# Optimization experiments

Hardware: AMD Instinct MI355X
Metric: run time of the kernel (lower is better)

The kernel has to match this reference:

```python
import jax, jax.numpy as jnp
import numpy as np

B, T, H, N = 4, 512, 32, 64
D = H * N  # n_embd = 2048


def setup_inputs() -> dict:
    key = jax.random.key(0)
    ks = jax.random.split(key, 8)
    f = lambda kk: jax.random.normal(kk, (B, T, H, N), dtype=jnp.float32)
    r = f(ks[0])
    w = f(ks[1])
    k = f(ks[2])
    v = f(ks[3])
    iclr = f(ks[4])
    # int8-style quantized output projection: int values in [-128,127] + per-row scale
    w_out_q = jax.random.randint(ks[5], (D, D), -128, 128, dtype=jnp.int32)
    w_out_scale = jax.random.uniform(ks[6], (D,), dtype=jnp.float32) * 0.01
    return {"r": r, "w": w, "k": k, "v": v, "iclr": iclr,
            "w_out_q": w_out_q, "w_out_scale": w_out_scale}


def _wkv7(r, w, k, v, iclr):
    """RWKV x070 WKV scan. All inputs [B,T,H,N]; returns [B,T,H*N]."""
    decay = jnp.exp(-jnp.exp(w))  # per-channel decay in (0,1), x070 parameterization
    # kk = l2-normalized key direction; a = -kk (removal), b = kk * sigmoid(iclr) (write)
    kk = k * jax.lax.rsqrt(jnp.sum(k * k, axis=-1, keepdims=True) + 1e-12)
    a = -kk
    b = kk * jax.nn.sigmoid(iclr)

    def step(state, inp):
        # state: [B,H,N,N]; each inp element: [B,H,N]
        r_t, d_t, k_t, v_t, a_t, b_t = inp
        sa = jnp.einsum('bhij,bhj->bhi', state, a_t)
        state = (state * d_t[:, :, None, :]
                 + sa[..., None] * b_t[:, :, None, :]
                 + v_t[..., None] * k_t[:, :, None, :])
        y_t = jnp.einsum('bhij,bhj->bhi', state, r_t)
        return state, y_t

    tb = lambda x: jnp.swapaxes(x, 0, 1)  # [B,T,H,N] -> [T,B,H,N]
    state0 = jnp.zeros((B, H, N, N), dtype=r.dtype)
    _, y = jax.lax.scan(step, state0, (tb(r), tb(decay), tb(k), tb(v), tb(a), tb(b)))
    return jnp.swapaxes(y, 0, 1).reshape(B, T, H * N)


def reference(r, w, k, v, iclr, w_out_q, w_out_scale):
    y = _wkv7(r, w, k, v, iclr)               # [B,T,D]
    # inline dequant of quantized output projection (per-output-row scale)
    W = w_out_q.astype(jnp.float32) * w_out_scale[:, None]  # [D,D]
    return jnp.einsum('btd,od->bto', y, W)    # [B,T,D]
```

## Files before the change

### kernel.cpp

```cpp
#include <hip/hip_runtime.h>
#include <hip/hip_bf16.h>
#include <stdint.h>

#define B_ 4
#define T_ 512
#define H_ 32
#define N_ 64
#define D_ 2048
#define M_ (B_*T_)

typedef __attribute__((ext_vector_type(4))) float f32x4;
typedef __attribute__((ext_vector_type(8))) short short8;

template <int CTRL>
__device__ __forceinline__ float dpp_add(float x) {
    int t = __builtin_amdgcn_mov_dpp(__float_as_int(x), CTRL, 0xF, 0xF, true);
    return x + __int_as_float(t);
}
__device__ __forceinline__ float bfly16(float x) {
    x = dpp_add<0xB1>(x);
    x = dpp_add<0x4E>(x);
    x = dpp_add<0x141>(x);
    x = dpp_add<0x140>(x);
    return x;
}

__global__ __launch_bounds__(256) void conv_w(const int* __restrict__ q,
                                              __hip_bfloat16* __restrict__ o) {
    int i = (blockIdx.x * 256 + threadIdx.x) * 4;
    int4 qi = *(const int4*)(q + i);
    __hip_bfloat16 t[4];
    t[0] = __float2bfloat16((float)qi.x);
    t[1] = __float2bfloat16((float)qi.y);
    t[2] = __float2bfloat16((float)qi.z);
    t[3] = __float2bfloat16((float)qi.w);
    *(uint2*)(o + i) = *(uint2*)t;
}

__global__ __launch_bounds__(256) void precomp_t(
    const float* __restrict__ r, const float* __restrict__ w,
    const float* __restrict__ k, const float* __restrict__ v,
    const float* __restrict__ iclr,
    float* __restrict__ rT, float* __restrict__ kT, float* __restrict__ vT,
    float* __restrict__ decT, float* __restrict__ kkT, float* __restrict__ bbT) {
    int g = blockIdx.x * 4 + (threadIdx.x >> 6);
    int lane = threadIdx.x & 63;
    int b = g >> 14;
    int t = (g >> 5) & (T_ - 1);
    int h = g & 31;
    size_t si = (size_t)g * 64 + lane;
    size_t di = ((((size_t)b * H_ + h) * T_) + t) * 64 + lane;
    float rv = r[si], wv = w[si], kv = k[si], vv = v[si], av = iclr[si];
    float d = expf(-expf(wv));
    float ss = kv * kv;
#pragma unroll
    for (int m = 1; m < 64; m <<= 1) ss += __shfl_xor(ss, m, 64);
    float kkv = kv * rsqrtf(ss + 1e-12f);
    float bbv = kkv * (1.f / (1.f + expf(-av)));
    rT[di] = rv; kT[di] = kv; vT[di] = vv;
    decT[di] = d; kkT[di] = kkv; bbT[di] = bbv;
}

__device__ __forceinline__ void gld4(const float* g, float* l) {
    __builtin_amdgcn_global_load_lds(
        (const __attribute__((address_space(1))) unsigned int*)g,
        (__attribute__((address_space(3))) unsigned int*)l, 4, 0, 0);
}

__global__ __launch_bounds__(64, 2) void wkv_scan(
    const float* __restrict__ rT, const float* __restrict__ kT,
    const float* __restrict__ vT, const float* __restrict__ decT,
    const float* __restrict__ kkT, const float* __restrict__ bbT,
    __hip_bfloat16* __restrict__ y) {
    const int bh = blockIdx.x & 127;
    const int wv = blockIdx.x >> 7;
    const int b = bh >> 5, h = bh & 31;
    const int lane = threadIdx.x;
    const int jg = lane & 15;
    const int rl = lane >> 4;
    const int row = wv * 4 + rl;
    const int jb = jg * 4;

    __shared__ float ring[8][6][64];

    const size_t sbase = (size_t)bh * T_ * 64;
    const float* st[6] = { rT + sbase, kT + sbase, vT + sbase,
                           decT + sbase, kkT + sbase, bbT + sbase };

#pragma unroll
    for (int i = 0; i < 8; ++i)
#pragma unroll
        for (int s = 0; s < 6; ++s)
            gld4(st[s] + i * 64 + lane, &ring[i][s][0]);

    float S[4] = {0.f, 0.f, 0.f, 0.f};

    for (int t = 0; t < T_; ++t) {
        const int slot = t & 7;
        asm volatile("s_waitcnt vmcnt(42)" ::: "memory");

        f32x4 Rc = *(const f32x4*)(&ring[slot][0][jb]);
        f32x4 Kc = *(const f32x4*)(&ring[slot][1][jb]);
        float vcv =                  ring[slot][2][row];
        f32x4 Dc = *(const f32x4*)(&ring[slot][3][jb]);
        f32x4 Ac = *(const f32x4*)(&ring[slot][4][jb]);
        f32x4 Bc = *(const f32x4*)(&ring[slot][5][jb]);

        float s01 = fmaf(S[1], Ac[1], S[0] * Ac[0]);
        float s23 = fmaf(S[3], Ac[3], S[2] * Ac[2]);
        const float sa = -bfly16(s01 + s23);

        float t0 = fmaf(sa, Bc[0], vcv * Kc[0]);
        S[0] = fmaf(S[0], Dc[0], t0);
        float t1 = fmaf(sa, Bc[1], vcv * Kc[1]);
        S[1] = fmaf(S[1], Dc[1], t1);
        float y01 = fmaf(S[1], Rc[1], S[0] * Rc[0]);
        float t2 = fmaf(sa, Bc[2], vcv * Kc[2]);
        S[2] = fmaf(S[2], Dc[2], t2);
        float t3 = fmaf(sa, Bc[3], vcv * Kc[3]);
        S[3] = fmaf(S[3], Dc[3], t3);
        float y23 = fmaf(S[3], Rc[3], S[2] * Rc[2]);
        float ys = bfly16(y01 + y23);
        if (jg == 0)
            y[((size_t)b * T_ + t) * D_ + h * 64 + row] = __float2bfloat16(ys);

        asm volatile("" ::: "memory");
        int tp = t + 8; if (tp > T_ - 1) tp = T_ - 1;
#pragma unroll
        for (int s = 0; s < 6; ++s)
            gld4(st[s] + (size_t)tp * 64 + lane, &ring[slot][s][0]);
    }
}

__device__ __forceinline__ void gload_lds16(const __hip_bfloat16* g, ushort* l) {
    __builtin_amdgcn_global_load_lds(
        (const __attribute__((address_space(1))) unsigned int*)g,
        (__attribute__((address_space(3))) unsigned int*)l, 16, 0, 0);
}

__global__ __launch_bounds__(256, 1) void gemm_bt(
    const __hip_bfloat16* __restrict__ A,
    const __hip_bfloat16* __restrict__ Bq,
    const float* __restrict__ scale,
    float* __restrict__ C) {
    const int K = D_;
    __shared__ __align__(16) ushort As[128 * 64];
    __shared__ __align__(16) ushort Bs[128 * 64];

    const int tid = threadIdx.x;
    const int lane = tid & 63;
    const int wave = tid >> 6;
    const int wr = wave >> 1, wc = wave & 1;
    const int m0 = blockIdx.x * 128;
    const int n0 = blockIdx.y * 128;

    const int srow8 = lane >> 3;
    const int scol8 = (lane & 7) * 8;
    const int ml = lane & 15;
    const int kq = (lane >> 4) * 8;

    f32x4 acc[4][4] = {};

    for (int k0 = 0; k0 < K; k0 += 64) {
#pragma unroll
        for (int c = 0; c < 4; ++c) {
            int rbase = wave * 32 + c * 8;
            int row = rbase + srow8;
            gload_lds16(A  + (size_t)(m0 + row) * K + k0 + scol8, &As[rbase * 64]);
            gload_lds16(Bq + (size_t)(n0 + row) * K + k0 + scol8, &Bs[rbase * 64]);
        }
        __syncthreads();
#pragma unroll
        for (int ks = 0; ks < 2; ++ks) {
            short8 af[4], bf[4];
#pragma unroll
            for (int tm = 0; tm < 4; ++tm)
                af[tm] = *(const short8*)(&As[(wr * 64 + tm * 16 + ml) * 64 + ks * 32 + kq]);
#pragma unroll
            for (int tn = 0; tn < 4; ++tn)
                bf[tn] = *(const short8*)(&Bs[(wc * 64 + tn * 16 + ml) * 64 + ks * 32 + kq]);
#pragma unroll
            for (int tm = 0; tm < 4; ++tm)
#pragma unroll
                for (int tn = 0; tn < 4; ++tn)
                    acc[tm][tn] = __builtin_amdgcn_mfma_f32_16x16x32_bf16(
                        af[tm], bf[tn], acc[tm][tn], 0, 0, 0);
        }
        __syncthreads();
    }

#pragma unroll
    for (int tn = 0; tn < 4; ++tn) {
        int gn = n0 + wc * 64 + tn * 16 + ml;
        float sc = scale[gn];
#pragma unroll
        for (int tm = 0; tm < 4; ++tm) {
            int gm = m0 + wr * 64 + tm * 16 + (lane >> 4) * 4;
#pragma unroll
            for (int rg = 0; rg < 4; ++rg)
                C[(size_t)(gm + rg) * D_ + gn] = acc[tm][tn][rg] * sc;
        }
    }
}

extern "C" void kernel_launch(void* const* d_in, const int* in_sizes, int n_in,
                              void* d_out, int out_size, void* d_ws, size_t ws_size,
                              hipStream_t stream) {
    (void)in_sizes; (void)n_in; (void)out_size; (void)ws_size;
    const float* r  = (const float*)d_in[0];
    const float* w  = (const float*)d_in[1];
    const float* k  = (const float*)d_in[2];
    const float* v  = (const float*)d_in[3];
    const float* ic = (const float*)d_in[4];
    const int*   wq = (const int*)d_in[5];
    const float* sc = (const float*)d_in[6];
    float* out = (float*)d_out;

    const size_t NE = (size_t)B_ * T_ * H_ * N_;
    char* p = (char*)d_ws;
    __hip_bfloat16* yb = (__hip_bfloat16*)p;  p += (size_t)M_ * D_ * 2;
    __hip_bfloat16* wb = (__hip_bfloat16*)p;  p += (size_t)D_ * D_ * 2;
    float* rT   = (float*)p;  p += NE * 4;
    float* kT   = (float*)p;  p += NE * 4;
    float* vT   = (float*)p;  p += NE * 4;
    float* decT = (float*)p;  p += NE * 4;
    float* kkT  = (float*)p;  p += NE * 4;
    float* bbT  = (float*)p;

    conv_w   <<<dim3((D_ * D_) / (256 * 4)), dim3(256), 0, stream>>>(wq, wb);
    precomp_t<<<dim3(B_ * T_ * H_ / 4), dim3(256), 0, stream>>>(
        r, w, k, v, ic, rT, kT, vT, decT, kkT, bbT);
    wkv_scan <<<dim3(B_ * H_ * 16), dim3(64), 0, stream>>>(
        rT, kT, vT, decT, kkT, bbT, yb);
    gemm_bt  <<<dim3(M_ / 128, D_ / 128), dim3(256), 0, stream>>>(yb, wb, sc, out);
}
```

Measured before the change: 352.8 us.

## Pack scan inputs interleaved per timestep and prefetch 4-step chunks with 16B loads

The six precomputed per-channel streams now go into one interleaved buffer laid out as [bh][t][6][64]. This lets the scan kernel fetch four timesteps per group with 16-byte global-to-LDS loads into a double-buffered ring, instead of issuing six 4-byte loads every step. The weight conversion kernel is merged into the prep kernel through extra blocks, which saves one launch. The prefetch distance shrinks from 8 steps to between 4 and 8, which could expose load latency in the serial scan.

```diff
diff --git a/kernel.cpp b/kernel.cpp
--- a/kernel.cpp
+++ b/kernel.cpp
@@ -25,31 +25,35 @@
     return x;
 }
 
-__global__ __launch_bounds__(256) void conv_w(const int* __restrict__ q,
-                                              __hip_bfloat16* __restrict__ o) {
-    int i = (blockIdx.x * 256 + threadIdx.x) * 4;
-    int4 qi = *(const int4*)(q + i);
-    __hip_bfloat16 t[4];
-    t[0] = __float2bfloat16((float)qi.x);
-    t[1] = __float2bfloat16((float)qi.y);
-    t[2] = __float2bfloat16((float)qi.z);
-    t[3] = __float2bfloat16((float)qi.w);
-    *(uint2*)(o + i) = *(uint2*)t;
-}
-
-__global__ __launch_bounds__(256) void precomp_t(
+__device__ __forceinline__ void gld16(const float* g, float* l) {
+    __builtin_amdgcn_global_load_lds(
+        (const __attribute__((address_space(1))) unsigned int*)g,
+        (__attribute__((address_space(3))) unsigned int*)l, 16, 0, 0);
+}
+
+__global__ __launch_bounds__(256) void prep(
     const float* __restrict__ r, const float* __restrict__ w,
     const float* __restrict__ k, const float* __restrict__ v,
-    const float* __restrict__ iclr,
-    float* __restrict__ rT, float* __restrict__ kT, float* __restrict__ vT,
-    float* __restrict__ decT, float* __restrict__ kkT, float* __restrict__ bbT) {
+    const float* __restrict__ iclr, const int* __restrict__ q,
+    float* __restrict__ pk, __hip_bfloat16* __restrict__ o) {
+    if (blockIdx.x >= 16384) {
+        int i = ((blockIdx.x - 16384) * 256 + threadIdx.x) * 4;
+        int4 qi = *(const int4*)(q + i);
+        __hip_bfloat16 t[4];
+        t[0] = __float2bfloat16((float)qi.x);
+        t[1] = __float2bfloat16((float)qi.y);
+        t[2] = __float2bfloat16((float)qi.z);
+        t[3] = __float2bfloat16((float)qi.w);
+        *(uint2*)(o + i) = *(uint2*)t;
+        return;
+    }
     int g = blockIdx.x * 4 + (threadIdx.x >> 6);
     int lane = threadIdx.x & 63;
     int b = g >> 14;
     int t = (g >> 5) & (T_ - 1);
     int h = g & 31;
     size_t si = (size_t)g * 64 + lane;
-    size_t di = ((((size_t)b * H_ + h) * T_) + t) * 64 + lane;
+    size_t di = (((size_t)(b * H_ + h) * T_) + t) * 384 + lane;
     float rv = r[si], wv = w[si], kv = k[si], vv = v[si], av = iclr[si];
     float d = expf(-expf(wv));
     float ss = kv * kv;
@@ -57,21 +61,16 @@
     for (int m = 1; m < 64; m <<= 1) ss += __shfl_xor(ss, m, 64);
     float kkv = kv * rsqrtf(ss + 1e-12f);
     float bbv = kkv * (1.f / (1.f + expf(-av)));
-    rT[di] = rv; kT[di] = kv; vT[di] = vv;
-    decT[di] = d; kkT[di] = kkv; bbT[di] = bbv;
-}
-
-__device__ __forceinline__ void gld4(const float* g, float* l) {
-    __builtin_amdgcn_global_load_lds(
-        (const __attribute__((address_space(1))) unsigned int*)g,
-        (__attribute__((address_space(3))) unsigned int*)l, 4, 0, 0);
+    pk[di          ] = rv;
+    pk[di + 1 * 64 ] = kv;
+    pk[di + 2 * 64 ] = vv;
+    pk[di + 3 * 64 ] = d;
+    pk[di + 4 * 64 ] = kkv;
+    pk[di + 5 * 64 ] = bbv;
 }
 
 __global__ __launch_bounds__(64, 2) void wkv_scan(
-    const float* __restrict__ rT, const float* __restrict__ kT,
-    const float* __restrict__ vT, const float* __restrict__ decT,
-    const float* __restrict__ kkT, const float* __restrict__ bbT,
-    __hip_bfloat16* __restrict__ y) {
+    const float* __restrict__ pk, __hip_bfloat16* __restrict__ y) {
     const int bh = blockIdx.x & 127;
     const int wv = blockIdx.x >> 7;
     const int b = bh >> 5, h = bh & 31;
@@ -79,56 +78,66 @@
     const int jg = lane & 15;
     const int rl = lane >> 4;
     const int row = wv * 4 + rl;
-    const int jb = jg * 4;
-
-    __shared__ float ring[8][6][64];
-
-    const size_t sbase = (size_t)bh * T_ * 64;
-    const float* st[6] = { rT + sbase, kT + sbase, vT + sbase,
-                           decT + sbase, kkT + sbase, bbT + sbase };
-
-#pragma unroll
-    for (int i = 0; i < 8; ++i)
-#pragma unroll
-        for (int s = 0; s < 6; ++s)
-            gld4(st[s] + i * 64 + lane, &ring[i][s][0]);
+
+    __shared__ __align__(16) float ring[2 * 1536];
+
+    const float* src = pk + (size_t)bh * T_ * 384;
+
+#pragma unroll
+    for (int gg = 0; gg < 2; ++gg) {
+        const float* g0 = src + (size_t)gg * 1536 + lane * 4;
+        float* l0 = &ring[gg * 1536];
+#pragma unroll
+        for (int c = 0; c < 6; ++c)
+            gld16(g0 + c * 256, l0 + c * 256);
+    }
 
     float S[4] = {0.f, 0.f, 0.f, 0.f};
 
-    for (int t = 0; t < T_; ++t) {
-        const int slot = t & 7;
-        asm volatile("s_waitcnt vmcnt(42)" ::: "memory");
-
-        f32x4 Rc = *(const f32x4*)(&ring[slot][0][jb]);
-        f32x4 Kc = *(const f32x4*)(&ring[slot][1][jb]);
-        float vcv =                  ring[slot][2][row];
-        f32x4 Dc = *(const f32x4*)(&ring[slot][3][jb]);
-        f32x4 Ac = *(const f32x4*)(&ring[slot][4][jb]);
-        f32x4 Bc = *(const f32x4*)(&ring[slot][5][jb]);
-
-        float s01 = fmaf(S[1], Ac[1], S[0] * Ac[0]);
-        float s23 = fmaf(S[3], Ac[3], S[2] * Ac[2]);
-        const float sa = -bfly16(s01 + s23);
-
-        float t0 = fmaf(sa, Bc[0], vcv * Kc[0]);
-        S[0] = fmaf(S[0], Dc[0], t0);
-        float t1 = fmaf(sa, Bc[1], vcv * Kc[1]);
-        S[1] = fmaf(S[1], Dc[1], t1);
-        float y01 = fmaf(S[1], Rc[1], S[0] * Rc[0]);
-        float t2 = fmaf(sa, Bc[2], vcv * Kc[2]);
-        S[2] = fmaf(S[2], Dc[2], t2);
-        float t3 = fmaf(sa, Bc[3], vcv * Kc[3]);
-        S[3] = fmaf(S[3], Dc[3], t3);
-        float y23 = fmaf(S[3], Rc[3], S[2] * Rc[2]);
-        float ys = bfly16(y01 + y23);
-        if (jg == 0)
-            y[((size_t)b * T_ + t) * D_ + h * 64 + row] = __float2bfloat16(ys);
+    for (int g = 0; g < T_ / 4; ++g) {
+        const int slot = g & 1;
+        if (g == 0) { asm volatile("s_waitcnt vmcnt(6)"  ::: "memory"); }
+        else        { asm volatile("s_waitcnt vmcnt(10)" ::: "memory"); }
+        const float* rb0 = &ring[slot * 1536];
+
+#pragma unroll
+        for (int i = 0; i < 4; ++i) {
+            const int t = g * 4 + i;
+            const float* rb = rb0 + i * 384;
+
+            f32x4 Rc = *(const f32x4*)(rb + 0 * 64 + jg * 4);
+            f32x4 Kc = *(const f32x4*)(rb + 1 * 64 + jg * 4);
+            float vcv =                 rb[2 * 64 + row];
+            f32x4 Dc = *(const f32x4*)(rb + 3 * 64 + jg * 4);
+            f32x4 Ac = *(const f32x4*)(rb + 4 * 64 + jg * 4);
+            f32x4 Bc = *(const f32x4*)(rb + 5 * 64 + jg * 4);
+
+            float s01 = fmaf(S[1], Ac[1], S[0] * Ac[0]);
+            float s23 = fmaf(S[3], Ac[3], S[2] * Ac[2]);
+            const float sa = -bfly16(s01 + s23);
+
+            float t0 = fmaf(sa, Bc[0], vcv * Kc[0]);
+            S[0] = fmaf(S[0], Dc[0], t0);
+            float t1 = fmaf(sa, Bc[1], vcv * Kc[1]);
+            S[1] = fmaf(S[1], Dc[1], t1);
+            float y01 = fmaf(S[1], Rc[1], S[0] * Rc[0]);
+            float t2 = fmaf(sa, Bc[2], vcv * Kc[2]);
+            S[2] = fmaf(S[2], Dc[2], t2);
+            float t3 = fmaf(sa, Bc[3], vcv * Kc[3]);
+            S[3] = fmaf(S[3], Dc[3], t3);
+            float y23 = fmaf(S[3], Rc[3], S[2] * Rc[2]);
+            float ys = bfly16(y01 + y23);
+            if (jg == 0)
+                y[((size_t)b * T_ + t) * D_ + h * 64 + row] = __float2bfloat16(ys);
+        }
 
         asm volatile("" ::: "memory");
-        int tp = t + 8; if (tp > T_ - 1) tp = T_ - 1;
-#pragma unroll
-        for (int s = 0; s < 6; ++s)
-            gld4(st[s] + (size_t)tp * 64 + lane, &ring[slot][s][0]);
+        int gp = g + 2; if (gp > T_ / 4 - 1) gp = T_ / 4 - 1;
+        const float* g0 = src + (size_t)gp * 1536 + lane * 4;
+        float* l0 = &ring[slot * 1536];
+#pragma unroll
+        for (int c = 0; c < 6; ++c)
+            gld16(g0 + c * 256, l0 + c * 256);
     }
 }
 
@@ -216,21 +225,12 @@
     const float* sc = (const float*)d_in[6];
     float* out = (float*)d_out;
 
-    const size_t NE = (size_t)B_ * T_ * H_ * N_;
     char* p = (char*)d_ws;
     __hip_bfloat16* yb = (__hip_bfloat16*)p;  p += (size_t)M_ * D_ * 2;
     __hip_bfloat16* wb = (__hip_bfloat16*)p;  p += (size_t)D_ * D_ * 2;
-    float* rT   = (float*)p;  p += NE * 4;
-    float* kT   = (float*)p;  p += NE * 4;
-    float* vT   = (float*)p;  p += NE * 4;
-    float* decT = (float*)p;  p += NE * 4;
-    float* kkT  = (float*)p;  p += NE * 4;
-    float* bbT  = (float*)p;
-
-    conv_w   <<<dim3((D_ * D_) / (256 * 4)), dim3(256), 0, stream>>>(wq, wb);
-    precomp_t<<<dim3(B_ * T_ * H_ / 4), dim3(256), 0, stream>>>(
-        r, w, k, v, ic, rT, kT, vT, decT, kkT, bbT);
-    wkv_scan <<<dim3(B_ * H_ * 16), dim3(64), 0, stream>>>(
-        rT, kT, vT, decT, kkT, bbT, yb);
-    gemm_bt  <<<dim3(M_ / 128, D_ / 128), dim3(256), 0, stream>>>(yb, wb, sc, out);
-}
+    float* pk = (float*)p;
+
+    prep    <<<dim3(16384 + 4096), dim3(256), 0, stream>>>(r, w, k, v, ic, wq, pk, wb);
+    wkv_scan<<<dim3(B_ * H_ * 16), dim3(64), 0, stream>>>(pk, yb);
+    gemm_bt <<<dim3(M_ / 128, D_ / 128), dim3(256), 0, stream>>>(yb, wb, sc, out);
+}
```

Result: faster. 299.2 us (-15.2%).
